# Performance work log

Measured on AMD Instinct MI355X. Metric: run time of the kernel, lower is better.

Reference implementation:

```python
import jax, jax.numpy as jnp
import numpy as np

B, I, H, R = 8192, 1024, 1024, 16  # batch, input_size, hidden_size, subspace_size


def setup_inputs() -> dict:
    key = jax.random.key(0)
    ks = jax.random.split(key, 11)
    s_in = 1.0 / np.sqrt(I)
    s_h = 1.0 / np.sqrt(H)
    return {
        "x": jax.random.normal(ks[0], (B, I), jnp.float32),
        "h0": jax.random.normal(ks[1], (B, H), jnp.float32),
        "c0": jax.random.normal(ks[2], (B, H), jnp.float32),
        # stacked per-gate params, gate order: [i, f, g, o]
        "W_i": jax.random.normal(ks[3], (4, H, I), jnp.float32) * s_in,
        "W_h": jax.random.normal(ks[4], (4, H, H), jnp.float32) * s_h,
        "b_i": jnp.zeros((4, H), jnp.float32),
        "b_h": jnp.zeros((4, H), jnp.float32),
        "A_i": jax.random.normal(ks[5], (4, R, I), jnp.float32),
        "B_i": jax.random.normal(ks[6], (4, H, R), jnp.float32) * 0.01,
        "A_h": jax.random.normal(ks[7], (4, R, H), jnp.float32),
        "B_h": jax.random.normal(ks[8], (4, H, R), jnp.float32) * 0.01,
    }


def reference(x, h0, c0, W_i, W_h, b_i, b_h, A_i, B_i, A_h, B_h):
    # Pre-activation for all 4 gates at once: [B, 4, H]
    pre = (
        jnp.einsum("bi,ghi->bgh", x, W_i)
        + jnp.einsum("bk,ghk->bgh", h0, W_h)
        + b_i[None, :, :]
        + b_h[None, :, :]
        # LoRA: x @ (B@A).T == (x @ A.T) @ B.T, done in factored (efficient) form
        + jnp.einsum("bgr,ghr->bgh", jnp.einsum("bi,gri->bgr", x, A_i), B_i)
        + jnp.einsum("bgr,ghr->bgh", jnp.einsum("bk,grk->bgr", h0, A_h), B_h)
    )
    i_t = jax.nn.sigmoid(pre[:, 0])
    f_t = jax.nn.sigmoid(pre[:, 1])
    g_t = jnp.tanh(pre[:, 2])
    o_t = jax.nn.sigmoid(pre[:, 3])
    c_t = f_t * c0 + i_t * g_t
    h_t = o_t * jnp.tanh(c_t)
    return (h_t, c_t)
```

## Files before the change

kernel.cpp:

```cpp
#include <hip/hip_runtime.h>
#include <hip/hip_bf16.h>
#include <cstdint>

#define B_  8192
#define I_  1024
#define H_  1024
#define R_  16
#define K_  2048
#define N_  4096

typedef __attribute__((ext_vector_type(4))) float f32x4;
typedef __attribute__((ext_vector_type(8))) __bf16 bf16x8;
typedef __attribute__((ext_vector_type(8))) unsigned short u16x8;
typedef __attribute__((ext_vector_type(4))) unsigned short u16x4;
typedef unsigned short u16;

__device__ __forceinline__ u16 f2bf(float f) {
  union { float f; unsigned u; } v; v.f = f;
  unsigned u = v.u;
  return (u16)((u + 0x7fffu + ((u >> 16) & 1u)) >> 16);
}

__device__ __forceinline__ float sigmoidf_(float x) {
  return 1.0f / (1.0f + __expf(-x));
}
__device__ __forceinline__ float tanhf_(float x) {
  return 1.0f - 2.0f / (__expf(2.0f * x) + 1.0f);
}

__global__ __launch_bounds__(256) void prep_all(
    const float* __restrict__ x, const float* __restrict__ h0,
    const float* __restrict__ W_i, const float* __restrict__ W_h,
    const float* __restrict__ b_i, const float* __restrict__ b_h,
    const float* __restrict__ A_i, const float* __restrict__ Bi,
    const float* __restrict__ A_h, const float* __restrict__ Bh,
    u16* __restrict__ Xc, u16* __restrict__ Wc, float* __restrict__ bc) {
  const int bid = blockIdx.x;
  const int tid = threadIdx.x;
  if (bid < 8192) {
    int idx = bid * 256 + tid;
    int e = idx << 3;
    int b = e >> 11;
    int k = e & (K_ - 1);
    const float* src = (k < I_) ? (x + ((size_t)b << 10) + k)
                                : (h0 + ((size_t)b << 10) + (k - I_));
    const f32x4 v0 = *(const f32x4*)src;
    const f32x4 v1 = *(const f32x4*)(src + 4);
    u16x8 o;
    o[0] = f2bf(v0[0]); o[1] = f2bf(v0[1]); o[2] = f2bf(v0[2]); o[3] = f2bf(v0[3]);
    o[4] = f2bf(v1[0]); o[5] = f2bf(v1[1]); o[6] = f2bf(v1[2]); o[7] = f2bf(v1[3]);
    *(u16x8*)(Xc + (size_t)e) = o;
  } else {
    const int gh = bid - 8192;
    const int g = gh >> 10, h = gh & (H_ - 1);
    float bi[R_], bh[R_];
#pragma unroll
    for (int r = 0; r < R_; ++r) {
      bi[r] = Bi[((size_t)(g * H_ + h) << 4) + r];
      bh[r] = Bh[((size_t)(g * H_ + h) << 4) + r];
    }
    u16* dst = Wc + (size_t)(h * 4 + g) * K_;
    const float* wi = W_i + ((size_t)(g * H_ + h) << 10);
    const float* wh = W_h + ((size_t)(g * H_ + h) << 10);
    const int k4 = tid * 4;
    f32x4 accI = *(const f32x4*)&wi[k4];
    f32x4 accH = *(const f32x4*)&wh[k4];
#pragma unroll
    for (int r = 0; r < R_; ++r) {
      const f32x4 ai = *(const f32x4*)&A_i[((size_t)(g * R_ + r) << 10) + k4];
      const f32x4 ah = *(const f32x4*)&A_h[((size_t)(g * R_ + r) << 10) + k4];
      accI += bi[r] * ai;
      accH += bh[r] * ah;
    }
    u16x4 oi, oh;
#pragma unroll
    for (int j = 0; j < 4; ++j) { oi[j] = f2bf(accI[j]); oh[j] = f2bf(accH[j]); }
    *(u16x4*)(dst + k4) = oi;
    *(u16x4*)(dst + I_ + k4) = oh;
    if (tid == 0) bc[h * 4 + g] = b_i[g * H_ + h] + b_h[g * H_ + h];
  }
}

#define BM 256
#define BN 256
#define BK 64
#define NT (K_ / BK)

#define GLOAD_LDS16(gp, lp)                                                        \
  __builtin_amdgcn_global_load_lds(                                                \
      (const __attribute__((address_space(1))) void*)(gp),                         \
      (__attribute__((address_space(3))) void*)(lp), 16, 0, 0)

#define BAR()                                                                      \
  do { asm volatile("" ::: "memory"); __builtin_amdgcn_s_barrier();                \
       asm volatile("" ::: "memory"); } while (0)

#define BARL()                                                                     \
  do { asm volatile("s_waitcnt lgkmcnt(0)" ::: "memory");                          \
       __builtin_amdgcn_s_barrier(); asm volatile("" ::: "memory"); } while (0)

#define WAITV0() asm volatile("s_waitcnt vmcnt(0)" ::: "memory")
#define WAITV6() asm volatile("s_waitcnt vmcnt(6)" ::: "memory")

#define AH(HI, SL) ((u16*)(lds_raw + ((HI) * 2 + (SL)) * 16384))
#define BH(HI, SL) ((u16*)(lds_raw + 65536 + ((HI) * 2 + (SL)) * 16384))

#define STAGE_H(GBASE, HALF, K0N, REGION)                                          \
  _Pragma("unroll")                                                                \
  for (int r_ = 0; r_ < 2; ++r_) {                                                 \
    int chunk_ = r_ * 512 + tid;                                                   \
    int rl_ = chunk_ >> 3, cp_ = chunk_ & 7;                                       \
    int cc_ = cp_ ^ (rl_ & 7);                                                     \
    GLOAD_LDS16((GBASE) + (size_t)((HALF) * 128 + rl_) * K_ + (K0N) + cc_ * 8,     \
                (char*)(REGION) + chunk_ * 16);                                    \
  }

#define READ_A(REGION)                                                             \
  _Pragma("unroll")                                                                \
  for (int mi_ = 0; mi_ < 4; ++mi_) {                                              \
    _Pragma("unroll")                                                              \
    for (int kk_ = 0; kk_ < 2; ++kk_) {                                            \
      const int rl_ = wave_m + mi_ * 16 + lr;                                      \
      av[mi_][kk_] = *(const bf16x8*)&(REGION)[rl_ * 64 +                          \
          (((kk_ * 4 + lk) ^ (rl_ & 7)) << 3)];                                    \
    }                                                                              \
  }

#define READ_B(REGION, BV)                                                         \
  _Pragma("unroll")                                                                \
  for (int nj_ = 0; nj_ < 2; ++nj_) {                                              \
    _Pragma("unroll")                                                              \
    for (int kk_ = 0; kk_ < 2; ++kk_) {                                            \
      const int rl_ = wave_n + nj_ * 16 + lr;                                      \
      BV[nj_][kk_] = *(const bf16x8*)&(REGION)[rl_ * 64 +                          \
          (((kk_ * 4 + lk) ^ (rl_ & 7)) << 3)];                                    \
    }                                                                              \
  }

#define MMA(MH, NH, BV)                                                            \
  do {                                                                             \
    __builtin_amdgcn_s_setprio(1);                                                 \
    _Pragma("unroll")                                                              \
    for (int mi_ = 0; mi_ < 4; ++mi_)                                              \
      _Pragma("unroll")                                                            \
      for (int nj_ = 0; nj_ < 2; ++nj_)                                            \
        _Pragma("unroll")                                                          \
        for (int kk_ = 0; kk_ < 2; ++kk_)                                          \
          acc[(MH) * 4 + mi_][(NH) * 2 + nj_] =                                    \
              __builtin_amdgcn_mfma_f32_16x16x32_bf16(                             \
                  av[mi_][kk_], BV[nj_][kk_],                                      \
                  acc[(MH) * 4 + mi_][(NH) * 2 + nj_], 0, 0, 0);                   \
    __builtin_amdgcn_s_setprio(0);                                                 \
  } while (0)

#define KTILE(CB, NB, T)                                                           \
  do {                                                                             \
    const int k1_ = ((T) + 1 < NT) ? ((T) + 1) * BK : 0;                           \
    const int k2_ = ((T) + 2 < NT) ? ((T) + 2) * BK : 0;                           \
    READ_A(AH(0, CB));                                                             \
    READ_B(BH(0, CB), bv0);                                                        \
    STAGE_H(Ag, 1, k1_, AH(1, NB));                                                \
    BAR(); MMA(0, 0, bv0); BAR();                                                  \
    READ_B(BH(1, CB), bv1);                                                        \
    STAGE_H(Bg, 0, k2_, BH(0, CB));                                                \
    BAR(); MMA(0, 1, bv1); BAR();                                                  \
    READ_A(AH(1, CB));                                                             \
    STAGE_H(Ag, 0, k2_, AH(0, CB));                                                \
    BAR(); MMA(1, 1, bv1); BAR();                                                  \
    STAGE_H(Bg, 1, k2_, BH(1, CB));                                                \
    WAITV6(); BAR(); MMA(1, 0, bv0); BAR();                                        \
  } while (0)

__global__ __launch_bounds__(512, 2) void lstm_gemm(
    const u16* __restrict__ Xc, const u16* __restrict__ Wc,
    const float* __restrict__ bc, const float* __restrict__ c0,
    float* __restrict__ out) {
  __shared__ __align__(16) char lds_raw[131072];

  const int tid = threadIdx.x;
  const int wave = tid >> 6, lane = tid & 63;
  const int lr = lane & 15, lk = lane >> 4;

  const int flat = blockIdx.y * gridDim.x + blockIdx.x;
  const int swz = (flat & 7) * 64 + (flat >> 3);
  const int bm = swz >> 4, bn = swz & 15;
  const int m0 = bm * BM, n0 = bn * BN;

  const int wave_m = (wave >> 2) * 64;
  const int wave_n = (wave & 3) * 32;

  f32x4 acc[8][4] = {};
  bf16x8 av[4][2], bv0[2][2], bv1[2][2];

  const u16* Ag = Xc + (size_t)m0 * K_;
  const u16* Bg = Wc + (size_t)n0 * K_;

  STAGE_H(Ag, 0, 0, AH(0, 0));
  STAGE_H(Bg, 0, 0, BH(0, 0));
  STAGE_H(Bg, 1, 0, BH(1, 0));
  STAGE_H(Ag, 1, 0, AH(1, 0));
  STAGE_H(Bg, 0, BK, BH(0, 1));
  STAGE_H(Ag, 0, BK, AH(0, 1));
  STAGE_H(Bg, 1, BK, BH(1, 1));
  WAITV6();
  BAR();

#pragma unroll 1
  for (int tt = 0; tt < NT; tt += 2) {
    KTILE(0, 1, tt);
    KTILE(1, 0, tt + 1);
  }

  WAITV0();
  float* lE = (float*)lds_raw;
  float biasv[4];
#pragma unroll
  for (int an = 0; an < 4; ++an)
    biasv[an] = bc[n0 + (an >> 1) * 128 + wave_n + (an & 1) * 16 + lr];

#pragma unroll
  for (int half = 0; half < 2; ++half) {
    BARL();
#pragma unroll
    for (int mi = 0; mi < 4; ++mi)
#pragma unroll
      for (int an = 0; an < 4; ++an)
#pragma unroll
        for (int j = 0; j < 4; ++j) {
          const int row = wave_m + mi * 16 + lk * 4 + j;
          const int col = (an >> 1) * 128 + wave_n + (an & 1) * 16 + lr;
          const int colx = col ^ ((((row & 3) ^ ((row >> 2) & 3))) << 4);
          lE[row * 256 + colx] = acc[half * 4 + mi][an][j] + biasv[an];
        }
    BARL();
#pragma unroll
    for (int jj = 0; jj < 4; ++jj) {
      const int item = jj * 512 + tid;
      const int hl4 = item & 15;
      const int rr = item >> 4;
      const int xorv = ((rr & 3) ^ ((rr >> 2) & 3)) << 4;
      const int grow = m0 + half * 128 + rr;
      const int hg = (n0 >> 2) + hl4 * 4;
      const f32x4 c0v = *(const f32x4*)&c0[(size_t)grow * H_ + hg];
      f32x4 htv, ctv;
#pragma unroll
      for (int q = 0; q < 4; ++q) {
        const int colx = (hl4 * 16 + q * 4) ^ xorv;
        const f32x4 pre = *(const f32x4*)&lE[rr * 256 + colx];
        float ig = sigmoidf_(pre[0]);
        float fg = sigmoidf_(pre[1]);
        float gg = tanhf_(pre[2]);
        float og = sigmoidf_(pre[3]);
        float ct = fg * c0v[q] + ig * gg;
        htv[q] = og * tanhf_(ct);
        ctv[q] = ct;
      }
      *(f32x4*)&out[(size_t)grow * H_ + hg] = htv;
      *(f32x4*)&out[(size_t)(B_ * H_) + (size_t)grow * H_ + hg] = ctv;
    }
  }
}

extern "C" void kernel_launch(void* const* d_in, const int* in_sizes, int n_in,
                              void* d_out, int out_size, void* d_ws, size_t ws_size,
                              hipStream_t stream) {
  const float* x   = (const float*)d_in[0];
  const float* h0  = (const float*)d_in[1];
  const float* c0  = (const float*)d_in[2];
  const float* W_i = (const float*)d_in[3];
  const float* W_h = (const float*)d_in[4];
  const float* b_i = (const float*)d_in[5];
  const float* b_h = (const float*)d_in[6];
  const float* A_i = (const float*)d_in[7];
  const float* B_i = (const float*)d_in[8];
  const float* A_h = (const float*)d_in[9];
  const float* B_h = (const float*)d_in[10];
  float* out = (float*)d_out;

  char* ws = (char*)d_ws;
  u16*   Xc = (u16*)ws;
  u16*   Wc = (u16*)(ws + ((size_t)32 << 20));
  float* bc = (float*)(ws + ((size_t)48 << 20));

  prep_all<<<dim3(8192 + 4096), dim3(256), 0, stream>>>(
      x, h0, W_i, W_h, b_i, b_h, A_i, B_i, A_h, B_h, Xc, Wc, bc);
  lstm_gemm<<<dim3(N_ / BN, B_ / BM), dim3(512), 0, stream>>>(Xc, Wc, bc, c0, out);
}
```

Measured before the change: 170.2 us.

## Load A operand directly from global into registers, stage only B in LDS

The X (A) operand is no longer staged through LDS. Each wave loads its A fragments straight from global memory into registers with a two-register-set ping-pong, while only the weight tile (B) is double-buffered in LDS. This removes the A LDS traffic and most of the barriers in each k-tile, but A reads are no longer shared across waves, which raises global/L2 traffic. Each tile also ends with a full vmcnt(0) wait, exposing global latency and reducing overlap.

```diff
diff --git a/kernel.cpp b/kernel.cpp
--- a/kernel.cpp
+++ b/kernel.cpp
@@ -100,75 +100,66 @@
        __builtin_amdgcn_s_barrier(); asm volatile("" ::: "memory"); } while (0)
 
 #define WAITV0() asm volatile("s_waitcnt vmcnt(0)" ::: "memory")
-#define WAITV6() asm volatile("s_waitcnt vmcnt(6)" ::: "memory")
-
-#define AH(HI, SL) ((u16*)(lds_raw + ((HI) * 2 + (SL)) * 16384))
-#define BH(HI, SL) ((u16*)(lds_raw + 65536 + ((HI) * 2 + (SL)) * 16384))
-
-#define STAGE_H(GBASE, HALF, K0N, REGION)                                          \
+
+#define BH(HI, SL) ((u16*)(lds_raw + ((HI) * 2 + (SL)) * 16384))
+
+#define STAGE_B(HALF, K0N, SL)                                                     \
   _Pragma("unroll")                                                                \
   for (int r_ = 0; r_ < 2; ++r_) {                                                 \
     int chunk_ = r_ * 512 + tid;                                                   \
     int rl_ = chunk_ >> 3, cp_ = chunk_ & 7;                                       \
     int cc_ = cp_ ^ (rl_ & 7);                                                     \
-    GLOAD_LDS16((GBASE) + (size_t)((HALF) * 128 + rl_) * K_ + (K0N) + cc_ * 8,     \
-                (char*)(REGION) + chunk_ * 16);                                    \
-  }
-
-#define READ_A(REGION)                                                             \
+    GLOAD_LDS16(Bg + (size_t)((HALF) * 128 + rl_) * K_ + (K0N) + cc_ * 8,          \
+                (char*)(BH(HALF, SL)) + chunk_ * 16);                              \
+  }
+
+#define READ_BV(SL)                                                                \
   _Pragma("unroll")                                                                \
-  for (int mi_ = 0; mi_ < 4; ++mi_) {                                              \
+  for (int nj_ = 0; nj_ < 4; ++nj_) {                                              \
     _Pragma("unroll")                                                              \
     for (int kk_ = 0; kk_ < 2; ++kk_) {                                            \
-      const int rl_ = wave_m + mi_ * 16 + lr;                                      \
-      av[mi_][kk_] = *(const bf16x8*)&(REGION)[rl_ * 64 +                          \
+      const int rl_ = wave_n + (nj_ & 1) * 16 + lr;                                \
+      bv[nj_][kk_] = *(const bf16x8*)&(BH(nj_ >> 1, SL))[rl_ * 64 +                \
           (((kk_ * 4 + lk) ^ (rl_ & 7)) << 3)];                                    \
     }                                                                              \
   }
 
-#define READ_B(REGION, BV)                                                         \
+#define LOAD_A(MH, K0N, AV)                                                        \
   _Pragma("unroll")                                                                \
-  for (int nj_ = 0; nj_ < 2; ++nj_) {                                              \
+  for (int mi_ = 0; mi_ < 4; ++mi_)                                                \
     _Pragma("unroll")                                                              \
-    for (int kk_ = 0; kk_ < 2; ++kk_) {                                            \
-      const int rl_ = wave_n + nj_ * 16 + lr;                                      \
-      BV[nj_][kk_] = *(const bf16x8*)&(REGION)[rl_ * 64 +                          \
-          (((kk_ * 4 + lk) ^ (rl_ & 7)) << 3)];                                    \
-    }                                                                              \
-  }
-
-#define MMA(MH, NH, BV)                                                            \
+    for (int kk_ = 0; kk_ < 2; ++kk_)                                              \
+      AV[mi_][kk_] = *(const bf16x8*)(Aw +                                         \
+          (size_t)((MH) * 128 + mi_ * 16) * K_ + (K0N) + kk_ * 32);
+
+#define MMA32(MH, AV)                                                              \
   do {                                                                             \
     __builtin_amdgcn_s_setprio(1);                                                 \
     _Pragma("unroll")                                                              \
-    for (int mi_ = 0; mi_ < 4; ++mi_)                                              \
+    for (int kk_ = 0; kk_ < 2; ++kk_)                                              \
       _Pragma("unroll")                                                            \
-      for (int nj_ = 0; nj_ < 2; ++nj_)                                            \
+      for (int mi_ = 0; mi_ < 4; ++mi_)                                            \
         _Pragma("unroll")                                                          \
-        for (int kk_ = 0; kk_ < 2; ++kk_)                                          \
-          acc[(MH) * 4 + mi_][(NH) * 2 + nj_] =                                    \
+        for (int nj_ = 0; nj_ < 4; ++nj_)                                          \
+          acc[(MH) * 4 + mi_][nj_] =                                               \
               __builtin_amdgcn_mfma_f32_16x16x32_bf16(                             \
-                  av[mi_][kk_], BV[nj_][kk_],                                      \
-                  acc[(MH) * 4 + mi_][(NH) * 2 + nj_], 0, 0, 0);                   \
+                  AV[mi_][kk_], bv[nj_][kk_],                                      \
+                  acc[(MH) * 4 + mi_][nj_], 0, 0, 0);                              \
     __builtin_amdgcn_s_setprio(0);                                                 \
   } while (0)
 
 #define KTILE(CB, NB, T)                                                           \
   do {                                                                             \
     const int k1_ = ((T) + 1 < NT) ? ((T) + 1) * BK : 0;                           \
-    const int k2_ = ((T) + 2 < NT) ? ((T) + 2) * BK : 0;                           \
-    READ_A(AH(0, CB));                                                             \
-    READ_B(BH(0, CB), bv0);                                                        \
-    STAGE_H(Ag, 1, k1_, AH(1, NB));                                                \
-    BAR(); MMA(0, 0, bv0); BAR();                                                  \
-    READ_B(BH(1, CB), bv1);                                                        \
-    STAGE_H(Bg, 0, k2_, BH(0, CB));                                                \
-    BAR(); MMA(0, 1, bv1); BAR();                                                  \
-    READ_A(AH(1, CB));                                                             \
-    STAGE_H(Ag, 0, k2_, AH(0, CB));                                                \
-    BAR(); MMA(1, 1, bv1); BAR();                                                  \
-    STAGE_H(Bg, 1, k2_, BH(1, CB));                                                \
-    WAITV6(); BAR(); MMA(1, 0, bv0); BAR();                                        \
+    READ_BV(CB);                                                                   \
+    STAGE_B(0, k1_, NB);                                                           \
+    STAGE_B(1, k1_, NB);                                                           \
+    LOAD_A(1, (T) * BK, avB);                                                      \
+    MMA32(0, avA);                                                                 \
+    LOAD_A(0, k1_, avA);                                                           \
+    MMA32(1, avB);                                                                 \
+    WAITV0();                                                                      \
+    BAR();                                                                         \
   } while (0)
 
 __global__ __launch_bounds__(512, 2) void lstm_gemm(
@@ -190,19 +181,15 @@
   const int wave_n = (wave & 3) * 32;
 
   f32x4 acc[8][4] = {};
-  bf16x8 av[4][2], bv0[2][2], bv1[2][2];
-
-  const u16* Ag = Xc + (size_t)m0 * K_;
+  bf16x8 avA[4][2], avB[4][2], bv[4][2];
+
+  const u16* Aw = Xc + (size_t)(m0 + wave_m + lr) * K_ + lk * 8;
   const u16* Bg = Wc + (size_t)n0 * K_;
 
-  STAGE_H(Ag, 0, 0, AH(0, 0));
-  STAGE_H(Bg, 0, 0, BH(0, 0));
-  STAGE_H(Bg, 1, 0, BH(1, 0));
-  STAGE_H(Ag, 1, 0, AH(1, 0));
-  STAGE_H(Bg, 0, BK, BH(0, 1));
-  STAGE_H(Ag, 0, BK, AH(0, 1));
-  STAGE_H(Bg, 1, BK, BH(1, 1));
-  WAITV6();
+  STAGE_B(0, 0, 0);
+  STAGE_B(1, 0, 0);
+  LOAD_A(0, 0, avA);
+  WAITV0();
   BAR();
 
 #pragma unroll 1
@@ -211,7 +198,6 @@
     KTILE(1, 0, tt + 1);
   }
 
-  WAITV0();
   float* lE = (float*)lds_raw;
   float biasv[4];
 #pragma unroll
```

Measured after the change: 406.0 us. +138.5%, slower.
